# Optimization experiments

Measured on AMD Instinct MI355X. Metric: run time of the kernel, lower is better.

The kernel has to match this reference:

```python
import jax, jax.numpy as jnp
import numpy as np

K_SIZE = 5  # local window
PAD = K_SIZE // 2


def setup_inputs() -> dict:
    key = jax.random.key(0)
    k1, k2, k3, k4 = jax.random.split(key, 4)
    B, H, W, C = 8, 128, 128, 64
    heads, d = 4, 16  # intermediate_dim=64 split over 4 heads
    return {
        "main": jax.random.normal(k1, (B, H, W, C), dtype=jnp.float32),
        "ref": jax.random.normal(k2, (B, H, W, C), dtype=jnp.float32),
        "W_main": jax.random.normal(k3, (heads, C, d), dtype=jnp.float32) * (2.0 / C) ** 0.5,
        "W_ref": jax.random.normal(k4, (heads, C, d), dtype=jnp.float32) * (2.0 / C) ** 0.5,
    }


def reference(main, ref, W_main, W_ref):
    # 1x1 conv projections per head: [n, B, H, W, d]
    q = jnp.einsum('bhwc,ncd->nbhwd', main, W_main)
    k = jnp.einsum('bhwc,ncd->nbhwd', ref, W_ref)
    B, H, W = main.shape[0], main.shape[1], main.shape[2]
    # SAME zero padding as tf.image.extract_patches
    kp = jnp.pad(k, ((0, 0), (0, 0), (PAD, PAD), (PAD, PAD), (0, 0)))
    # Score against each of the k_size*k_size shifted neighbors (row-major di, dj
    # matching extract_patches + Reshape ordering), without materializing patches.
    scores = [
        jnp.sum(q * kp[:, :, di:di + H, dj:dj + W, :], axis=-1)
        for di in range(K_SIZE) for dj in range(K_SIZE)
    ]
    # Extra key: the (projected) main pixel itself, concatenated last.
    scores.append(jnp.sum(q * q, axis=-1))
    attn = jax.nn.softmax(jnp.stack(scores, axis=-1), axis=-1)  # [n,B,H,W,k*k+1]
    # aggregation_mode == 'average' over heads
    return jnp.mean(attn, axis=0)  # [B,H,W,k*k+1]
```

## Files before the change

kernel.cpp:

```cpp
#include <hip/hip_runtime.h>

#define Bn 8
#define Hn 128
#define Wn 128
#define Cn 64
#define Dn 16
#define NS 26
#define NPX (Bn * Hn * Wn)

#define KPW 132
#define KP_IMG (KPW * KPW)
#define NBORD 66560

#define WS_Q_OFF_B   16384
#define WS_KP_OFF_B  (WS_Q_OFF_B + 8 * NPX * 16)
#define WS_NEEDED    ((size_t)WS_KP_OFF_B + (size_t)64 * KP_IMG * 16)

typedef _Float16 h2    __attribute__((ext_vector_type(2)));
typedef _Float16 f16x8 __attribute__((ext_vector_type(8)));
typedef float    f32x4 __attribute__((ext_vector_type(4)));

__device__ __forceinline__ unsigned int pkf16(float a, float b) {
    return __builtin_bit_cast(unsigned int, __builtin_amdgcn_cvt_pkrtz(a, b));
}
__device__ __forceinline__ float dot2(unsigned int a, unsigned int b, float c) {
    return __builtin_amdgcn_fdot2(__builtin_bit_cast(h2, a),
                                  __builtin_bit_cast(h2, b), c, false);
}
__device__ __forceinline__ f16x8 pk8(float4 a, float4 b) {
    const uint4 u = make_uint4(pkf16(a.x, a.y), pkf16(a.z, a.w),
                               pkf16(b.x, b.y), pkf16(b.z, b.w));
    return __builtin_bit_cast(f16x8, u);
}

__global__ __launch_bounds__(256, 3)
void proj_fused(const float* __restrict__ mainp,
                const float* __restrict__ refp,
                const float* __restrict__ Wm,
                const float* __restrict__ Wr,
                uint2* __restrict__ wsQ2,
                uint2* __restrict__ kp2,
                uint4* __restrict__ kp4)
{
    __shared__ uint4 sW[1024];

    const int tid = threadIdx.x;
    const int wg  = blockIdx.x;
    const int sw  = ((wg & 7) << 8) | (wg >> 3);

    {
        const int idx = wg * 33 + tid;
        if (tid < 33 && idx < NBORD) {
            const int pb = idx / 1040;
            const int r  = idx - pb * 1040;
            int row, col;
            if (r < 528) { const int q = r / 132; row = (q < 2) ? q : 128 + q; col = r - q * 132; }
            else { const int r2 = r - 528; const int s = r2 & 3; row = 2 + (r2 >> 2); col = (s < 2) ? s : 128 + s; }
            kp4[(size_t)pb * KP_IMG + row * KPW + col] = make_uint4(0, 0, 0, 0);
        }
    }

    for (int e = tid; e < 1024; e += 256) {
        const int ty = e >> 9;
        const int h  = (e >> 7) & 3;
        const int kt = (e >> 6) & 1;
        const int l  = e & 63;
        const int dd = l & 15;
        const int cb = kt * 32 + ((l >> 4) << 3);
        const float* W = ty ? Wr : Wm;
        const float* base = W + h * (Cn * Dn) + dd;
        uint4 v;
        v.x = pkf16(base[(cb + 0) * Dn], base[(cb + 1) * Dn]);
        v.y = pkf16(base[(cb + 2) * Dn], base[(cb + 3) * Dn]);
        v.z = pkf16(base[(cb + 4) * Dn], base[(cb + 5) * Dn]);
        v.w = pkf16(base[(cb + 6) * Dn], base[(cb + 7) * Dn]);
        sW[e] = v;
    }

    const int lane = tid & 63;
    const int wv   = tid >> 6;
    const int gbase = sw * 64 + wv * 16;
    const int px16 = lane & 15;
    const int lg   = lane >> 4;

    const float* mrow = mainp + (size_t)(gbase + px16) * Cn + lg * 8;
    const float* rrow = refp  + (size_t)(gbase + px16) * Cn + lg * 8;
    const float4 m0 = *(const float4*)(mrow);
    const float4 m1 = *(const float4*)(mrow + 4);
    const float4 m2 = *(const float4*)(mrow + 32);
    const float4 m3 = *(const float4*)(mrow + 36);
    const float4 r0 = *(const float4*)(rrow);
    const float4 r1 = *(const float4*)(rrow + 4);
    const float4 r2 = *(const float4*)(rrow + 32);
    const float4 r3 = *(const float4*)(rrow + 36);

    __syncthreads();

    f16x8 bm[4][2], br[4][2];
#pragma unroll
    for (int h = 0; h < 4; ++h)
#pragma unroll
        for (int t = 0; t < 2; ++t) {
            bm[h][t] = __builtin_bit_cast(f16x8, sW[(h * 2 + t) * 64 + lane]);
            br[h][t] = __builtin_bit_cast(f16x8, sW[(8 + h * 2 + t) * 64 + lane]);
        }

    const f16x8 Am0 = pk8(m0, m1), Am1 = pk8(m2, m3);
    const f16x8 Ar0 = pk8(r0, r1), Ar1 = pk8(r2, r3);

    const int px = gbase + px16;
    const int bb = px >> 14;
    const int yy = (px & 16383) >> 7;
    const int xx = px & 127;
    const int o  = (yy + 2) * KPW + (xx + 2);
    const int halfsel  = lg >> 1;
    const int wordpair = lg & 1;

#pragma unroll
    for (int h = 0; h < 4; ++h) {
        f32x4 z = {0.f, 0.f, 0.f, 0.f};
        z = __builtin_amdgcn_mfma_f32_16x16x32_f16(bm[h][0], Am0, z, 0, 0, 0);
        z = __builtin_amdgcn_mfma_f32_16x16x32_f16(bm[h][1], Am1, z, 0, 0, 0);
        const int w = h * 2 + halfsel;
        wsQ2[(size_t)w * NPX * 2 + px * 2 + wordpair] =
            make_uint2(pkf16(z[0], z[1]), pkf16(z[2], z[3]));
    }
#pragma unroll
    for (int h = 0; h < 4; ++h) {
        f32x4 z = {0.f, 0.f, 0.f, 0.f};
        z = __builtin_amdgcn_mfma_f32_16x16x32_f16(br[h][0], Ar0, z, 0, 0, 0);
        z = __builtin_amdgcn_mfma_f32_16x16x32_f16(br[h][1], Ar1, z, 0, 0, 0);
        const int w = h * 2 + halfsel;
        kp2[((size_t)(w * 8 + bb) * KP_IMG + o) * 2 + wordpair] =
            make_uint2(pkf16(z[0], z[1]), pkf16(z[2], z[3]));
    }
}

__global__ __launch_bounds__(256, 4)
void attn_row(const uint4* __restrict__ wsQ,
              const uint4* __restrict__ kp,
              float* __restrict__ out)
{
    __shared__ unsigned int sP[4 * 64 * 13];

    const int tid  = threadIdx.x;
    const int lane = tid & 63;
    const int wv   = tid >> 6;
    const int head = __builtin_amdgcn_readfirstlane(wv);
    const int wg = blockIdx.x;
    const int sw = ((wg & 7) << 8) | (wg >> 3);
    const int b  = sw >> 8;
    const int y  = (sw >> 1) & 127;
    const int x0 = (sw & 1) * 64;
    const int pxf = (b * Hn + y) * Wn + x0 + lane;

    const uint4 qa = wsQ[(head * 2 + 0) * NPX + pxf];
    const uint4 qb = wsQ[(head * 2 + 1) * NPX + pxf];

    const uint4* klo = kp + ((head * 2 + 0) * 8 + b) * KP_IMG;
    const uint4* khi = kp + ((head * 2 + 1) * 8 + b) * KP_IMG;

    float sc[NS];
#pragma unroll
    for (int di = 0; di < 5; ++di) {
        const int p0 = (y + di) * KPW + x0 + lane;
        uint4 kl[5], kh[5];
#pragma unroll
        for (int dj = 0; dj < 5; ++dj) { kl[dj] = klo[p0 + dj]; kh[dj] = khi[p0 + dj]; }
#pragma unroll
        for (int dj = 0; dj < 5; ++dj) {
            float s0 = dot2(qa.x, kl[dj].x, 0.f);
            float s1 = dot2(qb.x, kh[dj].x, 0.f);
            s0 = dot2(qa.y, kl[dj].y, s0);
            s1 = dot2(qb.y, kh[dj].y, s1);
            s0 = dot2(qa.z, kl[dj].z, s0);
            s1 = dot2(qb.z, kh[dj].z, s1);
            s0 = dot2(qa.w, kl[dj].w, s0);
            s1 = dot2(qb.w, kh[dj].w, s1);
            sc[di * 5 + dj] = s0 + s1;
        }
    }
    {
        float s0 = dot2(qa.x, qa.x, 0.f);
        float s1 = dot2(qb.x, qb.x, 0.f);
        s0 = dot2(qa.y, qa.y, s0);
        s1 = dot2(qb.y, qb.y, s1);
        s0 = dot2(qa.z, qa.z, s0);
        s1 = dot2(qb.z, qb.z, s1);
        s0 = dot2(qa.w, qa.w, s0);
        s1 = dot2(qb.w, qb.w, s1);
        sc[25] = s0 + s1;
    }

    float mx = sc[0];
#pragma unroll
    for (int i = 1; i < NS; ++i) mx = fmaxf(mx, sc[i]);
    float ssum = 0.f;
#pragma unroll
    for (int i = 0; i < NS; ++i) { sc[i] = __expf(sc[i] - mx); ssum += sc[i]; }
    const float inv = 1.0f / ssum;
#pragma unroll
    for (int i = 0; i < NS; ++i) sc[i] *= inv;

    {
        unsigned int* myrow = sP + (wv * 64 + lane) * 13;
#pragma unroll
        for (int j = 0; j < 13; ++j) {
            const unsigned int ulo = (unsigned int)(sc[2 * j] * 65535.f + 0.5f);
            const unsigned int uhi = (unsigned int)(sc[2 * j + 1] * 65535.f + 0.5f);
            myrow[j] = ulo | (uhi << 16);
        }
    }
    __syncthreads();

    const size_t ob = ((size_t)(b * Hn + y) * Wn + x0) * NS;
    for (int idx = tid; idx < 64 * 13; idx += 256) {
        const int px = idx / 13;
        const int p  = idx - px * 13;
        const unsigned int u0 = sP[(0 * 64 + px) * 13 + p];
        const unsigned int u1 = sP[(1 * 64 + px) * 13 + p];
        const unsigned int u2 = sP[(2 * 64 + px) * 13 + p];
        const unsigned int u3 = sP[(3 * 64 + px) * 13 + p];
        const float lo = (float)((u0 & 0xffffu) + (u1 & 0xffffu) +
                                 (u2 & 0xffffu) + (u3 & 0xffffu));
        const float hi = (float)((u0 >> 16) + (u1 >> 16) + (u2 >> 16) + (u3 >> 16));
        const float k = 1.f / (4.f * 65535.f);
        *(float2*)(out + ob + (size_t)px * NS + 2 * p) = make_float2(lo * k, hi * k);
    }
}

#define TILE 8
#define HALO 12
#define NHALO (HALO * HALO)
#define PXW 36
__global__ void pack_weights(const float* __restrict__ Wm,
                             const float* __restrict__ Wr,
                             unsigned int* __restrict__ wp) {
    const int idx = blockIdx.x * 256 + threadIdx.x;
    if (idx < 2 * 4 * 32 * Dn) {
        const int t = idx >> 11;
        const int r = idx & 2047;
        const int h = r >> 9;
        const int m = (r >> 4) & 31;
        const int d = r & 15;
        const float* W = t ? Wr : Wm;
        wp[idx] = pkf16(W[h * (Cn * Dn) + (2 * m) * Dn + d],
                        W[h * (Cn * Dn) + (2 * m + 1) * Dn + d]);
    }
}
__global__ __launch_bounds__(256, 4)
void local_attn_fused_r4(const float* __restrict__ mainp,
                         const float* __restrict__ refp,
                         const unsigned int* __restrict__ wp,
                         float* __restrict__ out)
{
    __shared__ unsigned int sK[NHALO * PXW];
    const int tid  = threadIdx.x;
    const int lane = tid & 63;
    const int wv   = tid >> 6;
    const int head = __builtin_amdgcn_readfirstlane(wv);
    const int b    = blockIdx.z;
    const int y0   = blockIdx.y * TILE;
    const int x0   = blockIdx.x * TILE;
    const unsigned int* wmh = wp + head * (32 * Dn);
    const unsigned int* wrh = wp + 2048 + head * (32 * Dn);
    for (int p = lane; p < NHALO; p += 64) {
        const int hr = p / HALO;
        const int hc = p - hr * HALO;
        const int gy = y0 - 2 + hr;
        const int gx = x0 - 2 + hc;
        float acc[Dn];
#pragma unroll
        for (int d = 0; d < Dn; ++d) acc[d] = 0.f;
        if ((unsigned)gy < (unsigned)Hn && (unsigned)gx < (unsigned)Wn) {
            const float4* rp4 = (const float4*)(refp + (((size_t)b * Hn + gy) * Wn + gx) * Cn);
#pragma unroll
            for (int c4 = 0; c4 < Cn / 4; ++c4) {
                const float4 rv = rp4[c4];
                const unsigned int r01 = pkf16(rv.x, rv.y);
                const unsigned int r23 = pkf16(rv.z, rv.w);
                const unsigned int* w0 = wrh + (2 * c4) * Dn;
                const unsigned int* w1 = wrh + (2 * c4 + 1) * Dn;
#pragma unroll
                for (int d = 0; d < Dn; ++d) acc[d] = dot2(r01, w0[d], acc[d]);
#pragma unroll
                for (int d = 0; d < Dn; ++d) acc[d] = dot2(r23, w1[d], acc[d]);
            }
        }
        unsigned int pk[8];
#pragma unroll
        for (int j = 0; j < 8; ++j) pk[j] = pkf16(acc[2 * j], acc[2 * j + 1]);
        unsigned int* dst = sK + p * PXW + head * 8;
        *(uint4*)(dst)     = make_uint4(pk[0], pk[1], pk[2], pk[3]);
        *(uint4*)(dst + 4) = make_uint4(pk[4], pk[5], pk[6], pk[7]);
    }
    const int pr = lane >> 3;
    const int pc = lane & 7;
    const float4* mp4 = (const float4*)(mainp + (((size_t)b * Hn + (y0 + pr)) * Wn + (x0 + pc)) * Cn);
    float q[Dn];
#pragma unroll
    for (int d = 0; d < Dn; ++d) q[d] = 0.f;
#pragma unroll
    for (int c4 = 0; c4 < Cn / 4; ++c4) {
        const float4 mv = mp4[c4];
        const unsigned int m01 = pkf16(mv.x, mv.y);
        const unsigned int m23 = pkf16(mv.z, mv.w);
        const unsigned int* w0 = wmh + (2 * c4) * Dn;
        const unsigned int* w1 = wmh + (2 * c4 + 1) * Dn;
#pragma unroll
        for (int d = 0; d < Dn; ++d) q[d] = dot2(m01, w0[d], q[d]);
#pragma unroll
        for (int d = 0; d < Dn; ++d) q[d] = dot2(m23, w1[d], q[d]);
    }
    unsigned int qh[8];
#pragma unroll
    for (int j = 0; j < 8; ++j) qh[j] = pkf16(q[2 * j], q[2 * j + 1]);
    __syncthreads();
    float sc[NS];
#pragma unroll
    for (int di = 0; di < 5; ++di) {
#pragma unroll
        for (int dj = 0; dj < 5; ++dj) {
            const int h = (pr + di) * HALO + (pc + dj);
            const unsigned int* src = sK + h * PXW + head * 8;
            const uint4 ka = *(const uint4*)(src);
            const uint4 kb = *(const uint4*)(src + 4);
            float s;
            s = dot2(qh[0], ka.x, 0.f);
            s = dot2(qh[1], ka.y, s);
            s = dot2(qh[2], ka.z, s);
            s = dot2(qh[3], ka.w, s);
            s = dot2(qh[4], kb.x, s);
            s = dot2(qh[5], kb.y, s);
            s = dot2(qh[6], kb.z, s);
            s = dot2(qh[7], kb.w, s);
            sc[di * 5 + dj] = s;
        }
    }
    {
        float s = q[0] * q[0];
#pragma unroll
        for (int d = 1; d < Dn; ++d) s = fmaf(q[d], q[d], s);
        sc[25] = s;
    }
    float mx = sc[0];
#pragma unroll
    for (int i = 1; i < NS; ++i) mx = fmaxf(mx, sc[i]);
    float ssum = 0.f;
#pragma unroll
    for (int i = 0; i < NS; ++i) { sc[i] = __expf(sc[i] - mx); ssum += sc[i]; }
    const float inv = 1.0f / ssum;
#pragma unroll
    for (int i = 0; i < NS; ++i) sc[i] *= inv;
    __syncthreads();
    {
        unsigned int* myrow = sK + (wv * 64 + lane) * 14;
#pragma unroll
        for (int j = 0; j < 13; ++j) myrow[j] = pkf16(sc[2 * j], sc[2 * j + 1]);
    }
    __syncthreads();
    const unsigned short* sA = (const unsigned short*)sK;
    const size_t obase = (((size_t)b * Hn + y0) * Wn + x0) * NS;
    for (int idx = tid; idx < TILE * TILE * NS; idx += 256) {
        const int r   = idx / (TILE * NS);
        const int t   = idx - r * (TILE * NS);
        const int c   = t / NS;
        const int i   = t - c * NS;
        const int ppx = r * TILE + c;
        float acc = 0.f;
#pragma unroll
        for (int h = 0; h < 4; ++h)
            acc += (float)__builtin_bit_cast(_Float16, sA[(h * 64 + ppx) * 28 + i]);
        out[obase + (size_t)r * (Wn * NS) + t] = 0.25f * acc;
    }
}

extern "C" void kernel_launch(void* const* d_in, const int* in_sizes, int n_in,
                              void* d_out, int out_size, void* d_ws, size_t ws_size,
                              hipStream_t stream) {
    (void)in_sizes; (void)n_in; (void)out_size;
    const float* mainp = (const float*)d_in[0];
    const float* refp  = (const float*)d_in[1];
    const float* Wm    = (const float*)d_in[2];
    const float* Wr    = (const float*)d_in[3];
    float* out = (float*)d_out;

    if (ws_size >= WS_NEEDED) {
        uint4* wsQ  = (uint4*)((char*)d_ws + WS_Q_OFF_B);
        uint4* kp   = (uint4*)((char*)d_ws + WS_KP_OFF_B);
        proj_fused<<<2048, 256, 0, stream>>>(mainp, refp, Wm, Wr,
                                             (uint2*)wsQ, (uint2*)kp, kp);
        attn_row<<<2048, 256, 0, stream>>>(wsQ, kp, out);
    } else {
        unsigned int* wpk = (unsigned int*)d_ws;
        pack_weights<<<16, 256, 0, stream>>>(Wm, Wr, wpk);
        dim3 grid2(Wn / TILE, Hn / TILE, Bn);
        local_attn_fused_r4<<<grid2, 256, 0, stream>>>(mainp, refp, wpk, out);
    }
}
```

Baseline: 40.33 us.

## Fuse Q projection into attention kernel instead of round-tripping through workspace

Moves the query 1x1-conv projection out of the projection kernel and into the attention kernel. Each attention block now computes Q for its own 64 pixels with MFMA and stages it in shared memory. This drops the Q write to global workspace and its read back. In exchange, the attention kernel reloads and packs the main weights per block, needs an extra barrier and more LDS, and its occupancy hint drops from 4 to 3.

```diff
diff --git a/kernel.cpp b/kernel.cpp
--- a/kernel.cpp
+++ b/kernel.cpp
@@ -34,15 +34,12 @@
 }
 
 __global__ __launch_bounds__(256, 3)
-void proj_fused(const float* __restrict__ mainp,
-                const float* __restrict__ refp,
-                const float* __restrict__ Wm,
-                const float* __restrict__ Wr,
-                uint2* __restrict__ wsQ2,
-                uint2* __restrict__ kp2,
-                uint4* __restrict__ kp4)
+void proj_k(const float* __restrict__ refp,
+            const float* __restrict__ Wr,
+            uint2* __restrict__ kp2,
+            uint4* __restrict__ kp4)
 {
-    __shared__ uint4 sW[1024];
+    __shared__ uint4 sW[512];
 
     const int tid = threadIdx.x;
     const int wg  = blockIdx.x;
@@ -60,15 +57,13 @@
         }
     }
 
-    for (int e = tid; e < 1024; e += 256) {
-        const int ty = e >> 9;
-        const int h  = (e >> 7) & 3;
+    for (int e = tid; e < 512; e += 256) {
+        const int h  = e >> 7;
         const int kt = (e >> 6) & 1;
         const int l  = e & 63;
         const int dd = l & 15;
         const int cb = kt * 32 + ((l >> 4) << 3);
-        const float* W = ty ? Wr : Wm;
-        const float* base = W + h * (Cn * Dn) + dd;
+        const float* base = Wr + h * (Cn * Dn) + dd;
         uint4 v;
         v.x = pkf16(base[(cb + 0) * Dn], base[(cb + 1) * Dn]);
         v.y = pkf16(base[(cb + 2) * Dn], base[(cb + 3) * Dn]);
@@ -83,12 +78,7 @@
     const int px16 = lane & 15;
     const int lg   = lane >> 4;
 
-    const float* mrow = mainp + (size_t)(gbase + px16) * Cn + lg * 8;
-    const float* rrow = refp  + (size_t)(gbase + px16) * Cn + lg * 8;
-    const float4 m0 = *(const float4*)(mrow);
-    const float4 m1 = *(const float4*)(mrow + 4);
-    const float4 m2 = *(const float4*)(mrow + 32);
-    const float4 m3 = *(const float4*)(mrow + 36);
+    const float* rrow = refp + (size_t)(gbase + px16) * Cn + lg * 8;
     const float4 r0 = *(const float4*)(rrow);
     const float4 r1 = *(const float4*)(rrow + 4);
     const float4 r2 = *(const float4*)(rrow + 32);
@@ -96,16 +86,13 @@
 
     __syncthreads();
 
-    f16x8 bm[4][2], br[4][2];
+    f16x8 br[4][2];
 #pragma unroll
     for (int h = 0; h < 4; ++h)
 #pragma unroll
-        for (int t = 0; t < 2; ++t) {
-            bm[h][t] = __builtin_bit_cast(f16x8, sW[(h * 2 + t) * 64 + lane]);
-            br[h][t] = __builtin_bit_cast(f16x8, sW[(8 + h * 2 + t) * 64 + lane]);
-        }
-
-    const f16x8 Am0 = pk8(m0, m1), Am1 = pk8(m2, m3);
+        for (int t = 0; t < 2; ++t)
+            br[h][t] = __builtin_bit_cast(f16x8, sW[(h * 2 + t) * 64 + lane]);
+
     const f16x8 Ar0 = pk8(r0, r1), Ar1 = pk8(r2, r3);
 
     const int px = gbase + px16;
@@ -119,15 +106,6 @@
 #pragma unroll
     for (int h = 0; h < 4; ++h) {
         f32x4 z = {0.f, 0.f, 0.f, 0.f};
-        z = __builtin_amdgcn_mfma_f32_16x16x32_f16(bm[h][0], Am0, z, 0, 0, 0);
-        z = __builtin_amdgcn_mfma_f32_16x16x32_f16(bm[h][1], Am1, z, 0, 0, 0);
-        const int w = h * 2 + halfsel;
-        wsQ2[(size_t)w * NPX * 2 + px * 2 + wordpair] =
-            make_uint2(pkf16(z[0], z[1]), pkf16(z[2], z[3]));
-    }
-#pragma unroll
-    for (int h = 0; h < 4; ++h) {
-        f32x4 z = {0.f, 0.f, 0.f, 0.f};
         z = __builtin_amdgcn_mfma_f32_16x16x32_f16(br[h][0], Ar0, z, 0, 0, 0);
         z = __builtin_amdgcn_mfma_f32_16x16x32_f16(br[h][1], Ar1, z, 0, 0, 0);
         const int w = h * 2 + halfsel;
@@ -136,26 +114,74 @@
     }
 }
 
-__global__ __launch_bounds__(256, 4)
-void attn_row(const uint4* __restrict__ wsQ,
-              const uint4* __restrict__ kp,
-              float* __restrict__ out)
+__global__ __launch_bounds__(256, 3)
+void attn_row_fq(const float* __restrict__ mainp,
+                 const float* __restrict__ Wm,
+                 const uint4* __restrict__ kp,
+                 float* __restrict__ out)
 {
-    __shared__ unsigned int sP[4 * 64 * 13];
+    __shared__ __align__(16) unsigned int sA_[3328];
+    __shared__ __align__(16) unsigned int sQ[4 * 64 * 8];
 
     const int tid  = threadIdx.x;
     const int lane = tid & 63;
     const int wv   = tid >> 6;
-    const int head = __builtin_amdgcn_readfirstlane(wv);
     const int wg = blockIdx.x;
     const int sw = ((wg & 7) << 8) | (wg >> 3);
     const int b  = sw >> 8;
     const int y  = (sw >> 1) & 127;
     const int x0 = (sw & 1) * 64;
-    const int pxf = (b * Hn + y) * Wn + x0 + lane;
-
-    const uint4 qa = wsQ[(head * 2 + 0) * NPX + pxf];
-    const uint4 qb = wsQ[(head * 2 + 1) * NPX + pxf];
+
+    uint4* sW = (uint4*)sA_;
+    for (int e = tid; e < 512; e += 256) {
+        const int h  = e >> 7;
+        const int kt = (e >> 6) & 1;
+        const int l  = e & 63;
+        const int dd = l & 15;
+        const int cb = kt * 32 + ((l >> 4) << 3);
+        const float* base = Wm + h * (Cn * Dn) + dd;
+        uint4 v;
+        v.x = pkf16(base[(cb + 0) * Dn], base[(cb + 1) * Dn]);
+        v.y = pkf16(base[(cb + 2) * Dn], base[(cb + 3) * Dn]);
+        v.z = pkf16(base[(cb + 4) * Dn], base[(cb + 5) * Dn]);
+        v.w = pkf16(base[(cb + 6) * Dn], base[(cb + 7) * Dn]);
+        sW[e] = v;
+    }
+
+    const int px16 = lane & 15;
+    const int lg   = lane >> 4;
+    const float* mrow = mainp +
+        (size_t)((b * Hn + y) * Wn + x0 + wv * 16 + px16) * Cn + lg * 8;
+    const float4 m0 = *(const float4*)(mrow);
+    const float4 m1 = *(const float4*)(mrow + 4);
+    const float4 m2 = *(const float4*)(mrow + 32);
+    const float4 m3 = *(const float4*)(mrow + 36);
+
+    __syncthreads();
+
+    f16x8 bm[4][2];
+#pragma unroll
+    for (int h = 0; h < 4; ++h)
+#pragma unroll
+        for (int t = 0; t < 2; ++t)
+            bm[h][t] = __builtin_bit_cast(f16x8, sW[(h * 2 + t) * 64 + lane]);
+
+    const f16x8 Am0 = pk8(m0, m1), Am1 = pk8(m2, m3);
+    const int rr = lg;
+#pragma unroll
+    for (int h = 0; h < 4; ++h) {
+        f32x4 z = {0.f, 0.f, 0.f, 0.f};
+        z = __builtin_amdgcn_mfma_f32_16x16x32_f16(bm[h][0], Am0, z, 0, 0, 0);
+        z = __builtin_amdgcn_mfma_f32_16x16x32_f16(bm[h][1], Am1, z, 0, 0, 0);
+        *(uint2*)&sQ[(h * 64 + wv * 16 + px16) * 8 + rr * 2] =
+            make_uint2(pkf16(z[0], z[1]), pkf16(z[2], z[3]));
+    }
+
+    __syncthreads();
+
+    const int head = __builtin_amdgcn_readfirstlane(wv);
+    const uint4 qa = *(const uint4*)&sQ[(head * 64 + lane) * 8];
+    const uint4 qb = *(const uint4*)&sQ[(head * 64 + lane) * 8 + 4];
 
     const uint4* klo = kp + ((head * 2 + 0) * 8 + b) * KP_IMG;
     const uint4* khi = kp + ((head * 2 + 1) * 8 + b) * KP_IMG;
@@ -202,6 +228,7 @@
 #pragma unroll
     for (int i = 0; i < NS; ++i) sc[i] *= inv;
 
+    unsigned int* sP = sA_;
     {
         unsigned int* myrow = sP + (wv * 64 + lane) * 13;
 #pragma unroll
@@ -386,11 +413,9 @@
     float* out = (float*)d_out;
 
     if (ws_size >= WS_NEEDED) {
-        uint4* wsQ  = (uint4*)((char*)d_ws + WS_Q_OFF_B);
-        uint4* kp   = (uint4*)((char*)d_ws + WS_KP_OFF_B);
-        proj_fused<<<2048, 256, 0, stream>>>(mainp, refp, Wm, Wr,
-                                             (uint2*)wsQ, (uint2*)kp, kp);
-        attn_row<<<2048, 256, 0, stream>>>(wsQ, kp, out);
+        uint4* kpb = (uint4*)((char*)d_ws + WS_KP_OFF_B);
+        proj_k<<<2048, 256, 0, stream>>>(refp, Wr, (uint2*)kpb, kpb);
+        attn_row_fq<<<2048, 256, 0, stream>>>(mainp, Wm, kpb, out);
     } else {
         unsigned int* wpk = (unsigned int*)d_ws;
         pack_weights<<<16, 256, 0, stream>>>(Wm, Wr, wpk);
```

New measurement: 36.07 us (median of 2 runs). 10.6% less time.
